# Performance work log

Measured on AMD Instinct MI355X. Metric: run time of the kernel, lower is better.

## Reference

```python
import jax, jax.numpy as jnp
import numpy as np

D = 512        # embed_dim
H = 2048       # expert hidden (4*D)
E = 8          # num_experts
TOPK = 2       # num_experts_per_tok


def setup_inputs() -> dict:
    key = jax.random.key(0)
    ks = jax.random.split(key, 5)
    s = 0.02
    x = jax.random.normal(ks[0], (4, 8192, D), dtype=jnp.float32)
    gate_w = jax.random.normal(ks[1], (D, E), dtype=jnp.float32) * s
    W1 = jax.random.normal(ks[2], (E, D, H), dtype=jnp.float32) * s
    W3 = jax.random.normal(ks[3], (E, D, H), dtype=jnp.float32) * s
    W2 = jax.random.normal(ks[4], (E, H, D), dtype=jnp.float32) * s
    return {"x": x, "gate_w": gate_w, "W1": W1, "W2": W2, "W3": W3}


def reference(x, gate_w, W1, W2, W3):
    B, S, _ = x.shape
    xt = x.reshape(-1, D)                      # [T, D]
    T = xt.shape[0]
    gate_logits = xt @ gate_w                  # [T, E]
    w, idx = jax.lax.top_k(gate_logits, TOPK)  # [T, k]
    w = jax.nn.softmax(w, axis=1).astype(xt.dtype)
    # combine weights: comb[t, e] = routing weight of expert e for token t (0 if unselected)
    comb = jnp.zeros((T, E), dtype=xt.dtype).at[jnp.arange(T)[:, None], idx].add(w)
    out = jnp.zeros_like(xt)
    for e in range(E):
        h = jax.nn.silu(xt @ W1[e]) * (xt @ W3[e])   # [T, H]
        out = out + (h @ W2[e]) * comb[:, e:e + 1]
    return out.reshape(B, S, D)
```

## Files before the change

kernel.cpp:

```cpp
#include <hip/hip_runtime.h>
#include <stdint.h>

#define D_DIM 512
#define H_DIM 2048
#define E_NUM 8
#define TOPK_N 2

typedef __attribute__((ext_vector_type(8))) short bf16x8;
typedef __attribute__((ext_vector_type(4))) float f32x4;

#define GLOAD_LDS16(gsrc, ldst)                                                     \
    __builtin_amdgcn_global_load_lds(                                               \
        (const __attribute__((address_space(1))) void*)(gsrc),                      \
        (__attribute__((address_space(3))) void*)(ldst), 16, 0, 0)

#define WAITVM(N) asm volatile("s_waitcnt vmcnt(" #N ")" ::: "memory")
#define SCB() __builtin_amdgcn_sched_barrier(0)
#define BAR() __builtin_amdgcn_s_barrier()

static __device__ __forceinline__ unsigned short f2bf(float f) {
    unsigned u = __float_as_uint(f);
    unsigned r = (u + 0x7fffu + ((u >> 16) & 1u)) >> 16;
    return (unsigned short)r;
}

__global__ void init_kernel(int* list_token, float* list_w, unsigned short* zrow, int cap) {
    int id = blockIdx.x * blockDim.x + threadIdx.x;
    if (id < cap) { list_token[id] = -1; list_w[id] = 0.f; }
    if (id < D_DIM) zrow[id] = 0;
}

__global__ void gwt_kernel(const float* __restrict__ gw, float* __restrict__ gwT) {
    int id = blockIdx.x * blockDim.x + threadIdx.x;
    int e = id >> 9, d = id & 511;
    gwT[id] = gw[d * E_NUM + e];
}

__global__ void gate_cvt_kernel(const float* __restrict__ x, const float* __restrict__ gwT,
                                unsigned short* __restrict__ xb,
                                int* __restrict__ ridx, float* __restrict__ rw, int T) {
    int wave = threadIdx.x >> 6;
    int lane = threadIdx.x & 63;
    int t = blockIdx.x * 4 + wave;
    if (t >= T) return;
    const float* xr = x + (size_t)t * D_DIM + lane * 8;
    float4 a = *(const float4*)xr;
    float4 b = *(const float4*)(xr + 4);
    union { unsigned short s[8]; uint4 v; } o;
    o.s[0] = f2bf(a.x); o.s[1] = f2bf(a.y); o.s[2] = f2bf(a.z); o.s[3] = f2bf(a.w);
    o.s[4] = f2bf(b.x); o.s[5] = f2bf(b.y); o.s[6] = f2bf(b.z); o.s[7] = f2bf(b.w);
    *(uint4*)(xb + (size_t)t * D_DIM + lane * 8) = o.v;
    float acc[8];
#pragma unroll
    for (int e = 0; e < 8; ++e) {
        const float* g = gwT + e * D_DIM + lane * 8;
        float4 g0 = *(const float4*)g;
        float4 g1 = *(const float4*)(g + 4);
        acc[e] = a.x * g0.x + a.y * g0.y + a.z * g0.z + a.w * g0.w
               + b.x * g1.x + b.y * g1.y + b.z * g1.z + b.w * g1.w;
    }
#pragma unroll
    for (int off = 32; off > 0; off >>= 1) {
#pragma unroll
        for (int e = 0; e < 8; ++e) acc[e] += __shfl_xor(acc[e], off, 64);
    }
    if (lane == 0) {
        int e0 = 0; float l0 = acc[0];
#pragma unroll
        for (int e = 1; e < 8; ++e) if (acc[e] > l0) { l0 = acc[e]; e0 = e; }
        int e1 = -1; float l1 = -1e30f;
#pragma unroll
        for (int e = 0; e < 8; ++e) if (e != e0 && acc[e] > l1) { l1 = acc[e]; e1 = e; }
        float w0 = 1.f / (1.f + expf(l1 - l0));
        ridx[t * 2] = e0; ridx[t * 2 + 1] = e1;
        rw[t * 2] = w0;  rw[t * 2 + 1] = 1.f - w0;
    }
}

__global__ void tconv_kernel(const float* __restrict__ in, unsigned short* __restrict__ out,
                             int R, int C) {
    __shared__ float tile[32][33];
    int e = blockIdx.z;
    const float* src = in + (size_t)e * R * C;
    unsigned short* dst = out + (size_t)e * R * C;
    int c = blockIdx.x * 32 + threadIdx.x;
#pragma unroll
    for (int i = 0; i < 4; ++i) {
        int r = blockIdx.y * 32 + threadIdx.y + i * 8;
        tile[threadIdx.y + i * 8][threadIdx.x] = src[(size_t)r * C + c];
    }
    __syncthreads();
    int r2 = blockIdx.y * 32 + threadIdx.x;
#pragma unroll
    for (int i = 0; i < 4; ++i) {
        int c2 = blockIdx.x * 32 + threadIdx.y + i * 8;
        dst[(size_t)c2 * R + r2] = f2bf(tile[threadIdx.x][threadIdx.y + i * 8]);
    }
}

__global__ void hist_kernel(const int* __restrict__ ridx, int* __restrict__ partial, int npairs) {
    __shared__ int cnt[E_NUM];
    if (threadIdx.x < E_NUM) cnt[threadIdx.x] = 0;
    __syncthreads();
    for (int i = blockIdx.x * blockDim.x + threadIdx.x; i < npairs; i += gridDim.x * blockDim.x)
        atomicAdd(&cnt[ridx[i]], 1);
    __syncthreads();
    if (threadIdx.x < E_NUM) partial[blockIdx.x * E_NUM + threadIdx.x] = cnt[threadIdx.x];
}

__global__ void scan_kernel(const int* __restrict__ partial, int* __restrict__ seg,
                            int* __restrict__ block_base) {
    __shared__ int sp[64 * E_NUM];
    __shared__ int segl[E_NUM + 1];
    int tid = threadIdx.x;
    if (tid < 64 * E_NUM) sp[tid] = partial[tid];
    __syncthreads();
    if (tid == 0) {
        int off = 0;
        for (int e = 0; e < E_NUM; ++e) {
            segl[e] = off;
            int c = 0;
            for (int b = 0; b < 64; ++b) c += sp[b * E_NUM + e];
            off += (c + 127) & ~127;
        }
        segl[E_NUM] = off;
    }
    __syncthreads();
    if (tid < E_NUM) {
        int run = segl[tid];
        for (int b = 0; b < 64; ++b) { block_base[b * E_NUM + tid] = run; run += sp[b * E_NUM + tid]; }
        seg[tid] = segl[tid];
        if (tid == 0) seg[E_NUM] = segl[E_NUM];
    }
}

__global__ void scatter_kernel(const int* __restrict__ ridx, const float* __restrict__ rw,
                               const int* __restrict__ block_base,
                               int* __restrict__ list_token, float* __restrict__ list_w, int npairs) {
    __shared__ int base[E_NUM];
    __shared__ int cnt[E_NUM];
    if (threadIdx.x < E_NUM) { base[threadIdx.x] = block_base[blockIdx.x * E_NUM + threadIdx.x]; cnt[threadIdx.x] = 0; }
    __syncthreads();
    for (int i = blockIdx.x * blockDim.x + threadIdx.x; i < npairs; i += gridDim.x * blockDim.x) {
        int e = ridx[i];
        int pos = base[e] + atomicAdd(&cnt[e], 1);
        list_token[pos] = i >> 1;
        list_w[pos] = rw[i];
    }
}

__global__ __launch_bounds__(256) void gemm1_kernel(
    const unsigned short* __restrict__ xb,
    const unsigned short* __restrict__ w1t,
    const unsigned short* __restrict__ w3t,
    const unsigned short* __restrict__ zrow,
    const int* __restrict__ list_token,
    const int* __restrict__ seg,
    unsigned short* __restrict__ hbuf,
    int chunk_base, int MT, int MG) {
    __shared__ short As[2][128 * 64];
    __shared__ short Bs[2][128 * 64];

    int bfl = blockIdx.x;
    int xcd = bfl & 7;
    int idx = bfl >> 3;
    int mlocal = idx % MG;
    int yt = idx / MG;
    int mt = mlocal * 8 + xcd;
    if (mt >= MT) return;

    int tid = threadIdx.x;
    int w = tid >> 6, l = tid & 63;
    int m0 = mt * 128;
    int slot0 = chunk_base + m0;
    int n0 = yt * 64;

    int e = 0;
#pragma unroll
    for (int i = 0; i < E_NUM - 1; ++i) if (slot0 >= seg[i + 1]) e = i + 1;
    const unsigned short* b1 = w1t + ((size_t)e * H_DIM + n0) * D_DIM;
    const unsigned short* b3 = w3t + ((size_t)e * H_DIM + n0) * D_DIM;

    int lr8 = l >> 3, p = l & 7;
    const unsigned short* aptr[4];
    const unsigned short* bptr[4];
#pragma unroll
    for (int q = 0; q < 4; ++q) {
        int row = (q * 4 + w) * 8 + lr8;
        int c = p ^ (row & 7);
        int tok = list_token[slot0 + row];
        aptr[q] = (tok >= 0 ? xb + (size_t)tok * D_DIM : zrow) + c * 8;
        bptr[q] = (row < 64 ? b1 + (size_t)row * D_DIM
                            : b3 + (size_t)(row - 64) * D_DIM) + c * 8;
    }

    int wm = (w & 1) * 64;
    int wn = (w >> 1) * 32;
    int lrr = l & 15;
    int lk = (l >> 4) * 8;

    f32x4 acc1[4][2] = {};
    f32x4 acc3[4][2] = {};

#define G1_STAGE(K0, BUF)                                                           \
    {                                                                               \
        _Pragma("unroll")                                                           \
        for (int q = 0; q < 4; ++q) {                                               \
            GLOAD_LDS16(aptr[q] + (K0), &As[BUF][(q * 4 + w) * 512]);               \
            GLOAD_LDS16(bptr[q] + (K0), &Bs[BUF][(q * 4 + w) * 512]);               \
        }                                                                           \
    }

#define G1_COMPUTE(BUF)                                                             \
    {                                                                               \
        _Pragma("unroll")                                                           \
        for (int ks = 0; ks < 64; ks += 32) {                                       \
            int cblk = (ks + lk) >> 3;                                              \
            bf16x8 af[4], b1f[2], b3f[2];                                           \
            _Pragma("unroll")                                                       \
            for (int i = 0; i < 4; ++i) {                                           \
                int row = wm + i * 16 + lrr;                                        \
                af[i] = *(const bf16x8*)&As[BUF][row * 64 + ((cblk ^ (row & 7)) << 3)]; \
            }                                                                       \
            _Pragma("unroll")                                                       \
            for (int j = 0; j < 2; ++j) {                                           \
                int r1 = wn + j * 16 + lrr;                                         \
                b1f[j] = *(const bf16x8*)&Bs[BUF][r1 * 64 + ((cblk ^ (r1 & 7)) << 3)]; \
                int r3 = 64 + wn + j * 16 + lrr;                                    \
                b3f[j] = *(const bf16x8*)&Bs[BUF][r3 * 64 + ((cblk ^ (r3 & 7)) << 3)]; \
            }                                                                       \
            __builtin_amdgcn_s_setprio(1);                                          \
            _Pragma("unroll")                                                       \
            for (int i = 0; i < 4; ++i)                                             \
                _Pragma("unroll")                                                   \
                for (int j = 0; j < 2; ++j) {                                       \
                    acc1[i][j] = __builtin_amdgcn_mfma_f32_16x16x32_bf16(af[i], b1f[j], acc1[i][j], 0, 0, 0); \
                    acc3[i][j] = __builtin_amdgcn_mfma_f32_16x16x32_bf16(af[i], b3f[j], acc3[i][j], 0, 0, 0); \
                }                                                                   \
            __builtin_amdgcn_s_setprio(0);                                          \
        }                                                                           \
    }

    G1_STAGE(0, 0);
    G1_STAGE(64, 1);
#pragma unroll
    for (int t = 0; t < 8; t += 2) {
        WAITVM(8);
        BAR();
        SCB();
        G1_COMPUTE(0);
        SCB();
        BAR();
        if (t + 2 < 8) G1_STAGE((t + 2) * 64, 0);
        if (t < 6) { WAITVM(8); } else { WAITVM(0); }
        BAR();
        SCB();
        G1_COMPUTE(1);
        SCB();
        BAR();
        if (t + 3 < 8) G1_STAGE((t + 3) * 64, 1);
    }
#undef G1_STAGE
#undef G1_COMPUTE

    int lrow0 = (l >> 4) * 4, lcol = l & 15;
#pragma unroll
    for (int i = 0; i < 4; ++i)
#pragma unroll
        for (int j = 0; j < 2; ++j)
#pragma unroll
            for (int r = 0; r < 4; ++r) {
                int row = wm + i * 16 + lrow0 + r;
                int col = wn + j * 16 + lcol;
                float v1 = acc1[i][j][r];
                float v3 = acc3[i][j][r];
                float h = v1 / (1.f + __expf(-v1)) * v3;
                hbuf[(size_t)(m0 + row) * H_DIM + n0 + col] = f2bf(h);
            }
}

__global__ __launch_bounds__(256) void gemm2_kernel(
    const unsigned short* __restrict__ hbuf,
    const unsigned short* __restrict__ w2t,
    const int* __restrict__ list_token,
    const float* __restrict__ list_w,
    const int* __restrict__ seg,
    float* __restrict__ out,
    int chunk_base, int MT) {
    __shared__ short As[2][128 * 64];
    __shared__ short Bs[2][128 * 64];

    int bfl = blockIdx.x;
    int xcd = bfl & 7;
    int idx = bfl >> 3;
    int yt = idx & 3;
    int mlocal = idx >> 2;
    int mt = mlocal * 8 + xcd;
    if (mt >= MT) return;

    int tid = threadIdx.x;
    int w = tid >> 6, l = tid & 63;
    int m0 = mt * 128;
    int slot0 = chunk_base + m0;
    int n0 = yt * 128;

    int e = 0;
#pragma unroll
    for (int i = 0; i < E_NUM - 1; ++i) if (slot0 >= seg[i + 1]) e = i + 1;
    const unsigned short* b2 = w2t + ((size_t)e * D_DIM + n0) * H_DIM;

    int lr8 = l >> 3, p = l & 7;
    const unsigned short* aptr[4];
    const unsigned short* bptr[4];
#pragma unroll
    for (int q = 0; q < 4; ++q) {
        int row = (q * 4 + w) * 8 + lr8;
        int c = p ^ (row & 7);
        aptr[q] = hbuf + (size_t)(m0 + row) * H_DIM + c * 8;
        bptr[q] = b2 + (size_t)row * H_DIM + c * 8;
    }

    int wm = (w & 1) * 64;
    int wn = (w >> 1) * 64;
    int lrr = l & 15;
    int lk = (l >> 4) * 8;

    f32x4 acc[4][4] = {};

#define G2_STAGE(K0, BUF)                                                           \
    {                                                                               \
        _Pragma("unroll")                                                           \
        for (int q = 0; q < 4; ++q) {                                               \
            GLOAD_LDS16(aptr[q] + (K0), &As[BUF][(q * 4 + w) * 512]);               \
            GLOAD_LDS16(bptr[q] + (K0), &Bs[BUF][(q * 4 + w) * 512]);               \
        }                                                                           \
    }

#define G2_COMPUTE(BUF)                                                             \
    {                                                                               \
        _Pragma("unroll")                                                           \
        for (int ks = 0; ks < 64; ks += 32) {                                       \
            int cblk = (ks + lk) >> 3;                                              \
            bf16x8 af[4], bf[4];                                                    \
            _Pragma("unroll")                                                       \
            for (int i = 0; i < 4; ++i) {                                           \
                int row = wm + i * 16 + lrr;                                        \
                af[i] = *(const bf16x8*)&As[BUF][row * 64 + ((cblk ^ (row & 7)) << 3)]; \
            }                                                                       \
            _Pragma("unroll")                                                       \
            for (int j = 0; j < 4; ++j) {                                           \
                int row = wn + j * 16 + lrr;                                        \
                bf[j] = *(const bf16x8*)&Bs[BUF][row * 64 + ((cblk ^ (row & 7)) << 3)]; \
            }                                                                       \
            __builtin_amdgcn_s_setprio(1);                                          \
            _Pragma("unroll")                                                       \
            for (int i = 0; i < 4; ++i)                                             \
                _Pragma("unroll")                                                   \
                for (int j = 0; j < 4; ++j)                                         \
                    acc[i][j] = __builtin_amdgcn_mfma_f32_16x16x32_bf16(af[i], bf[j], acc[i][j], 0, 0, 0); \
            __builtin_amdgcn_s_setprio(0);                                          \
        }                                                                           \
    }

    G2_STAGE(0, 0);
    G2_STAGE(64, 1);
    for (int t = 0; t < 30; t += 2) {
        WAITVM(8);
        BAR();
        SCB();
        G2_COMPUTE(0);
        SCB();
        BAR();
        G2_STAGE((t + 2) * 64, 0);
        WAITVM(8);
        BAR();
        SCB();
        G2_COMPUTE(1);
        SCB();
        BAR();
        G2_STAGE((t + 3) * 64, 1);
    }
    WAITVM(8);
    BAR();
    SCB();
    G2_COMPUTE(0);
    SCB();
    BAR();
    WAITVM(0);
    BAR();
    SCB();
    G2_COMPUTE(1);
    SCB();
    BAR();
#undef G2_STAGE
#undef G2_COMPUTE

    int lrow0 = (l >> 4) * 4, lcol = l & 15;
#pragma unroll
    for (int i = 0; i < 4; ++i)
#pragma unroll
        for (int r = 0; r < 4; ++r) {
            int row = wm + i * 16 + lrow0 + r;
            int tok = list_token[slot0 + row];
            if (tok < 0) continue;
            float wgt = list_w[slot0 + row];
#pragma unroll
            for (int j = 0; j < 4; ++j) {
                int col = wn + j * 16 + lcol;
                atomicAdd(&out[(size_t)tok * D_DIM + n0 + col], acc[i][j][r] * wgt);
            }
        }
}

extern "C" void kernel_launch(void* const* d_in, const int* in_sizes, int n_in,
                              void* d_out, int out_size, void* d_ws, size_t ws_size,
                              hipStream_t stream) {
    const float* x  = (const float*)d_in[0];
    const float* gw = (const float*)d_in[1];
    const float* W1 = (const float*)d_in[2];
    const float* W2 = (const float*)d_in[3];
    const float* W3 = (const float*)d_in[4];
    float* out = (float*)d_out;

    int T = in_sizes[0] / D_DIM;
    int npairs = T * TOPK_N;
    const int CAP = npairs + E_NUM * 128;
    const int NCHUNK = 4;
    int chunk_slots = CAP / NCHUNK;
    int MT = chunk_slots / 128;
    int MG = (MT + 7) / 8;

    char* p = (char*)d_ws;
    size_t off = 0;
    auto take = [&](size_t bytes) {
        char* r = p + off;
        off = (off + bytes + 255) & ~(size_t)255;
        return r;
    };
    int* seg           = (int*)take((E_NUM + 1) * 4);
    int* partial       = (int*)take(64 * E_NUM * 4);
    int* block_base    = (int*)take(64 * E_NUM * 4);
    int* list_token    = (int*)take((size_t)CAP * 4);
    float* list_w      = (float*)take((size_t)CAP * 4);
    int* ridx          = (int*)take((size_t)npairs * 4);
    float* rw          = (float*)take((size_t)npairs * 4);
    float* gwT         = (float*)take((size_t)E_NUM * D_DIM * 4);
    unsigned short* zrow = (unsigned short*)take((size_t)D_DIM * 2);
    unsigned short* xb  = (unsigned short*)take((size_t)T * D_DIM * 2);
    unsigned short* w1t = (unsigned short*)take((size_t)E_NUM * D_DIM * H_DIM * 2);
    unsigned short* w3t = (unsigned short*)take((size_t)E_NUM * D_DIM * H_DIM * 2);
    unsigned short* w2t = (unsigned short*)take((size_t)E_NUM * D_DIM * H_DIM * 2);
    unsigned short* hbuf = (unsigned short*)take((size_t)chunk_slots * H_DIM * 2);
    (void)ws_size;

    hipMemsetAsync(d_out, 0, (size_t)out_size * sizeof(float), stream);

    init_kernel<<<(CAP + 255) / 256, 256, 0, stream>>>(list_token, list_w, zrow, CAP);
    gwt_kernel<<<(E_NUM * D_DIM) / 256, 256, 0, stream>>>(gw, gwT);

    gate_cvt_kernel<<<T / 4, 256, 0, stream>>>(x, gwT, xb, ridx, rw, T);

    dim3 tb(32, 8);
    tconv_kernel<<<dim3(H_DIM / 32, D_DIM / 32, E_NUM), tb, 0, stream>>>(W1, w1t, D_DIM, H_DIM);
    tconv_kernel<<<dim3(H_DIM / 32, D_DIM / 32, E_NUM), tb, 0, stream>>>(W3, w3t, D_DIM, H_DIM);
    tconv_kernel<<<dim3(D_DIM / 32, H_DIM / 32, E_NUM), tb, 0, stream>>>(W2, w2t, H_DIM, D_DIM);

    hist_kernel<<<64, 256, 0, stream>>>(ridx, partial, npairs);
    scan_kernel<<<1, 512, 0, stream>>>(partial, seg, block_base);
    scatter_kernel<<<64, 256, 0, stream>>>(ridx, rw, block_base, list_token, list_w, npairs);

    int g1_grid = 8 * MG * (H_DIM / 64);
    int g2_grid = 8 * MG * (D_DIM / 128);
    for (int c = 0; c < NCHUNK; ++c) {
        int cb = c * chunk_slots;
        gemm1_kernel<<<g1_grid, 256, 0, stream>>>(
            xb, w1t, w3t, zrow, list_token, seg, hbuf, cb, MT, MG);
        gemm2_kernel<<<g2_grid, 256, 0, stream>>>(
            hbuf, w2t, list_token, list_w, seg, out, cb, MT);
    }
}
```

Baseline: 956.0 us.

## Widen gemm2 to full-D tiles with triple buffering and one launch per phase

Each gemm2 block now computes a 128×512 output tile, covering the whole embed dimension, with 512 threads and a K-step of 32. It uses a three-stage LDS ring with a new swizzle, so the A (hbuf) tile is loaded once instead of four times across column tiles. The host now sizes hbuf to hold all routed slots when the workspace allows. It runs every gemm1 chunk first and then a single gemm2 launch per phase, cutting launches and the gemm1/gemm2 ping-pong. The costs are much higher LDS use (around 120KB, which allows only one block per CU), 128 accumulator registers per thread, and a larger hbuf footprint.

```diff
diff --git a/kernel.cpp b/kernel.cpp
--- a/kernel.cpp
+++ b/kernel.cpp
@@ -279,7 +279,7 @@
             }
 }
 
-__global__ __launch_bounds__(256) void gemm2_kernel(
+__global__ __launch_bounds__(512, 2) void gemm2_kernel(
     const unsigned short* __restrict__ hbuf,
     const unsigned short* __restrict__ w2t,
     const int* __restrict__ list_token,
@@ -287,14 +287,12 @@
     const int* __restrict__ seg,
     float* __restrict__ out,
     int chunk_base, int MT) {
-    __shared__ short As[2][128 * 64];
-    __shared__ short Bs[2][128 * 64];
+    __shared__ __align__(16) short As[3][128 * 32];
+    __shared__ __align__(16) short Bs[3][512 * 32];
 
     int bfl = blockIdx.x;
     int xcd = bfl & 7;
-    int idx = bfl >> 3;
-    int yt = idx & 3;
-    int mlocal = idx >> 2;
+    int mlocal = bfl >> 3;
     int mt = mlocal * 8 + xcd;
     if (mt >= MT) return;
 
@@ -302,96 +300,89 @@
     int w = tid >> 6, l = tid & 63;
     int m0 = mt * 128;
     int slot0 = chunk_base + m0;
-    int n0 = yt * 128;
 
     int e = 0;
 #pragma unroll
     for (int i = 0; i < E_NUM - 1; ++i) if (slot0 >= seg[i + 1]) e = i + 1;
-    const unsigned short* b2 = w2t + ((size_t)e * D_DIM + n0) * H_DIM;
-
-    int lr8 = l >> 3, p = l & 7;
-    const unsigned short* aptr[4];
-    const unsigned short* bptr[4];
+    const unsigned short* b2 = w2t + (size_t)e * D_DIM * H_DIM;
+
+    int gsrc8 = ((l & 3) ^ ((l >> 3) & 3)) * 8;
+    int arow = w * 16 + (l >> 2);
+    const unsigned short* pa = hbuf + (size_t)(m0 + arow) * H_DIM + gsrc8;
+    const unsigned short* pb[4];
 #pragma unroll
     for (int q = 0; q < 4; ++q) {
-        int row = (q * 4 + w) * 8 + lr8;
-        int c = p ^ (row & 7);
-        aptr[q] = hbuf + (size_t)(m0 + row) * H_DIM + c * 8;
-        bptr[q] = b2 + (size_t)row * H_DIM + c * 8;
+        int brow = w * 64 + q * 16 + (l >> 2);
+        pb[q] = b2 + (size_t)brow * H_DIM + gsrc8;
     }
 
     int wm = (w & 1) * 64;
-    int wn = (w >> 1) * 64;
+    int wn = (w >> 1) * 128;
     int lrr = l & 15;
-    int lk = (l >> 4) * 8;
-
-    f32x4 acc[4][4] = {};
-
-#define G2_STAGE(K0, BUF)                                                           \
+    int gq = l >> 4;
+    int aoff[4], boff[8];
+#pragma unroll
+    for (int i = 0; i < 4; ++i) {
+        int row = wm + i * 16 + lrr;
+        aoff[i] = row * 64 + ((gq ^ ((row >> 1) & 3)) << 4);
+    }
+#pragma unroll
+    for (int j = 0; j < 8; ++j) {
+        int row = wn + j * 16 + lrr;
+        boff[j] = row * 64 + ((gq ^ ((row >> 1) & 3)) << 4);
+    }
+
+    f32x4 acc[4][8] = {};
+
+#define G2_STAGE(KO, SBUF)                                                          \
     {                                                                               \
-        _Pragma("unroll")                                                           \
-        for (int q = 0; q < 4; ++q) {                                               \
-            GLOAD_LDS16(aptr[q] + (K0), &As[BUF][(q * 4 + w) * 512]);               \
-            GLOAD_LDS16(bptr[q] + (K0), &Bs[BUF][(q * 4 + w) * 512]);               \
-        }                                                                           \
+        GLOAD_LDS16(pa + (KO), &As[SBUF][(w * 16) * 32]);                           \
+        _Pragma("unroll")                                                           \
+        for (int q = 0; q < 4; ++q)                                                 \
+            GLOAD_LDS16(pb[q] + (KO), &Bs[SBUF][(w * 64 + q * 16) * 32]);           \
     }
 
 #define G2_COMPUTE(BUF)                                                             \
     {                                                                               \
-        _Pragma("unroll")                                                           \
-        for (int ks = 0; ks < 64; ks += 32) {                                       \
-            int cblk = (ks + lk) >> 3;                                              \
-            bf16x8 af[4], bf[4];                                                    \
+        const char* Ab = (const char*)As[BUF];                                      \
+        const char* Bb = (const char*)Bs[BUF];                                      \
+        bf16x8 af[4], bfr[8];                                                       \
+        _Pragma("unroll")                                                           \
+        for (int i = 0; i < 4; ++i) af[i] = *(const bf16x8*)(Ab + aoff[i]);         \
+        _Pragma("unroll")                                                           \
+        for (int j = 0; j < 8; ++j) bfr[j] = *(const bf16x8*)(Bb + boff[j]);        \
+        __builtin_amdgcn_s_setprio(1);                                              \
+        _Pragma("unroll")                                                           \
+        for (int i = 0; i < 4; ++i)                                                 \
             _Pragma("unroll")                                                       \
-            for (int i = 0; i < 4; ++i) {                                           \
-                int row = wm + i * 16 + lrr;                                        \
-                af[i] = *(const bf16x8*)&As[BUF][row * 64 + ((cblk ^ (row & 7)) << 3)]; \
-            }                                                                       \
-            _Pragma("unroll")                                                       \
-            for (int j = 0; j < 4; ++j) {                                           \
-                int row = wn + j * 16 + lrr;                                        \
-                bf[j] = *(const bf16x8*)&Bs[BUF][row * 64 + ((cblk ^ (row & 7)) << 3)]; \
-            }                                                                       \
-            __builtin_amdgcn_s_setprio(1);                                          \
-            _Pragma("unroll")                                                       \
-            for (int i = 0; i < 4; ++i)                                             \
-                _Pragma("unroll")                                                   \
-                for (int j = 0; j < 4; ++j)                                         \
-                    acc[i][j] = __builtin_amdgcn_mfma_f32_16x16x32_bf16(af[i], bf[j], acc[i][j], 0, 0, 0); \
-            __builtin_amdgcn_s_setprio(0);                                          \
-        }                                                                           \
+            for (int j = 0; j < 8; ++j)                                             \
+                acc[i][j] = __builtin_amdgcn_mfma_f32_16x16x32_bf16(af[i], bfr[j], acc[i][j], 0, 0, 0); \
+        __builtin_amdgcn_s_setprio(0);                                              \
     }
 
     G2_STAGE(0, 0);
-    G2_STAGE(64, 1);
-    for (int t = 0; t < 30; t += 2) {
-        WAITVM(8);
-        BAR();
-        SCB();
+    G2_STAGE(32, 1);
+    for (int t = 0; t < 60; t += 3) {
+        WAITVM(5); BAR(); SCB();
+        G2_STAGE((t + 2) * 32, 2);
         G2_COMPUTE(0);
-        SCB();
-        BAR();
-        G2_STAGE((t + 2) * 64, 0);
-        WAITVM(8);
-        BAR();
-        SCB();
+        WAITVM(5); BAR(); SCB();
+        G2_STAGE((t + 3) * 32, 0);
         G2_COMPUTE(1);
-        SCB();
-        BAR();
-        G2_STAGE((t + 3) * 64, 1);
-    }
-    WAITVM(8);
-    BAR();
-    SCB();
+        WAITVM(5); BAR(); SCB();
+        G2_STAGE((t + 4) * 32, 1);
+        G2_COMPUTE(2);
+    }
+    WAITVM(5); BAR(); SCB();
+    G2_STAGE(62 * 32, 2);
     G2_COMPUTE(0);
-    SCB();
-    BAR();
-    WAITVM(0);
-    BAR();
-    SCB();
+    WAITVM(5); BAR(); SCB();
+    G2_STAGE(63 * 32, 0);
     G2_COMPUTE(1);
-    SCB();
-    BAR();
+    WAITVM(5); BAR(); SCB();
+    G2_COMPUTE(2);
+    WAITVM(0); BAR(); SCB();
+    G2_COMPUTE(0);
 #undef G2_STAGE
 #undef G2_COMPUTE
 
@@ -405,9 +396,9 @@
             if (tok < 0) continue;
             float wgt = list_w[slot0 + row];
 #pragma unroll
-            for (int j = 0; j < 4; ++j) {
+            for (int j = 0; j < 8; ++j) {
                 int col = wn + j * 16 + lcol;
-                atomicAdd(&out[(size_t)tok * D_DIM + n0 + col], acc[i][j][r] * wgt);
+                atomicAdd(&out[(size_t)tok * D_DIM + col], acc[i][j][r] * wgt);
             }
         }
 }
@@ -450,8 +441,11 @@
     unsigned short* w1t = (unsigned short*)take((size_t)E_NUM * D_DIM * H_DIM * 2);
     unsigned short* w3t = (unsigned short*)take((size_t)E_NUM * D_DIM * H_DIM * 2);
     unsigned short* w2t = (unsigned short*)take((size_t)E_NUM * D_DIM * H_DIM * 2);
-    unsigned short* hbuf = (unsigned short*)take((size_t)chunk_slots * H_DIM * 2);
-    (void)ws_size;
+
+    size_t hbuf_full = (size_t)CAP * H_DIM * 2;
+    int PH = (ws_size >= off + hbuf_full + 4096) ? 1 : 2;
+    int phase_slots = CAP / PH;
+    unsigned short* hbuf = (unsigned short*)take((size_t)phase_slots * H_DIM * 2);
 
     hipMemsetAsync(d_out, 0, (size_t)out_size * sizeof(float), stream);
 
@@ -470,12 +464,18 @@
     scatter_kernel<<<64, 256, 0, stream>>>(ridx, rw, block_base, list_token, list_w, npairs);
 
     int g1_grid = 8 * MG * (H_DIM / 64);
-    int g2_grid = 8 * MG * (D_DIM / 128);
-    for (int c = 0; c < NCHUNK; ++c) {
-        int cb = c * chunk_slots;
-        gemm1_kernel<<<g1_grid, 256, 0, stream>>>(
-            xb, w1t, w3t, zrow, list_token, seg, hbuf, cb, MT, MG);
-        gemm2_kernel<<<g2_grid, 256, 0, stream>>>(
-            hbuf, w2t, list_token, list_w, seg, out, cb, MT);
-    }
-}
+    int cpp = phase_slots / chunk_slots;
+    for (int ph = 0; ph < PH; ++ph) {
+        int pb = ph * phase_slots;
+        for (int c = 0; c < cpp; ++c) {
+            int cb = pb + c * chunk_slots;
+            gemm1_kernel<<<g1_grid, 256, 0, stream>>>(
+                xb, w1t, w3t, zrow, list_token, seg,
+                hbuf + (size_t)(c * chunk_slots) * H_DIM, cb, MT, MG);
+        }
+        int MT2 = phase_slots / 128;
+        int g2_grid = 8 * ((MT2 + 7) / 8);
+        gemm2_kernel<<<g2_grid, 512, 0, stream>>>(
+            hbuf, w2t, list_token, list_w, seg, out, pb, MT2);
+    }
+}
```

Measured after the change: 1.001 ms. 1.05x slower.
